# Performance work log

Hardware: AMD Instinct MI355X
Metric: run time of the kernel (lower is better)

The kernel has to match this reference:

```python
import jax, jax.numpy as jnp
import numpy as np


def _gcn_conv(x, W, b, src, dst, num_nodes):
    """PyG GCNConv: linear transform, add self-loops, symmetric norm, scatter-add."""
    h = x @ W  # [N, out] - transform first (cheaper gather on small dim)
    loop = jnp.arange(num_nodes, dtype=src.dtype)
    s = jnp.concatenate([src, loop])  # sources (message senders)
    d = jnp.concatenate([dst, loop])  # targets (aggregators)
    deg = jax.ops.segment_sum(jnp.ones_like(d, dtype=h.dtype), d, num_segments=num_nodes)
    dinv = jnp.where(deg > 0, jax.lax.rsqrt(deg), 0.0)
    norm = dinv[s] * dinv[d]  # [E+N]
    msg = h[s] * norm[:, None]  # gather + scale
    out = jax.ops.segment_sum(msg, d, num_segments=num_nodes)  # scatter-add
    return out + b


def setup_inputs() -> dict:
    key = jax.random.key(0)
    k1, k2, k3, k4 = jax.random.split(key, 4)
    N, F_IN, H, C, E = 100000, 128, 16, 7, 3200000
    x = jax.random.normal(k1, (N, F_IN), dtype=jnp.float32)
    edge_index = jax.random.randint(k2, (2, E), 0, N, dtype=jnp.int64)
    W1 = jax.random.normal(k3, (F_IN, H), dtype=jnp.float32) / np.sqrt(F_IN)
    b1 = jnp.zeros((H,), dtype=jnp.float32)
    W2 = jax.random.normal(k4, (H, C), dtype=jnp.float32) / np.sqrt(H)
    b2 = jnp.zeros((C,), dtype=jnp.float32)
    return {"x": x, "edge_index": edge_index, "W1": W1, "b1": b1, "W2": W2, "b2": b2}


def reference(x, edge_index, W1, b1, W2, b2):
    N = x.shape[0]
    src, dst = edge_index[0], edge_index[1]
    h = _gcn_conv(x, W1, b1, src, dst, N)
    h = jax.nn.relu(h)
    # dropout is identity in eval mode
    h = _gcn_conv(h, W2, b2, src, dst, N)
    return jax.nn.log_softmax(h, axis=1)
```

## Files before the change

### kernel.cpp

```cpp
#include <hip/hip_runtime.h>

#define BSHIFT 7
#define BNODES 128
#define BMASK 127
#define CAP 6144
#define PT 512
#define P_EPB (PT * 16)
#define TPB 256

__device__ __forceinline__ unsigned pkbf2(float a, float b) {
    unsigned ua = __float_as_uint(a), ub = __float_as_uint(b);
    ua = (ua + 0x7fffu + ((ua >> 16) & 1u)) >> 16;
    ub = (ub + 0x7fffu + ((ub >> 16) & 1u)) >> 16;
    return ua | (ub << 16);
}
__device__ __forceinline__ float bflo(unsigned u) { return __uint_as_float(u << 16); }
__device__ __forceinline__ float bfhi(unsigned u) { return __uint_as_float(u & 0xffff0000u); }

__global__ void detect_kernel(const unsigned int* __restrict__ w, int* __restrict__ flag,
                              int* __restrict__ gcur, int nb) {
    __shared__ int any;
    if (threadIdx.x == 0) any = 0;
    __syncthreads();
    int nz = 0;
    for (int k = threadIdx.x; k < 1024; k += blockDim.x)
        if (w[2 * k + 1] != 0u) nz = 1;
    if (nz) atomicOr(&any, 1);
    for (int i = threadIdx.x; i < nb; i += blockDim.x) gcur[i] = 0;
    __syncthreads();
    if (threadIdx.x == 0) *flag = (any == 0) ? 1 : 0;
}

__global__ __launch_bounds__(PT) void fused_place_gemm_kernel(
    const void* __restrict__ ei, const int* __restrict__ flag,
    int* __restrict__ gcur, unsigned* __restrict__ pairs,
    const float* __restrict__ x, const float* __restrict__ W1,
    float* __restrict__ hs, int E, int nb, int pb, int N) {
    __shared__ alignas(16) char smem[47120];
    int tid = threadIdx.x;
    if ((int)blockIdx.x < pb) {
        int* cnt  = (int*)smem;
        int* bbs  = (int*)(smem + 4096);
        int* cur  = (int*)(smem + 8208);
        int* ssum = (int*)(smem + 12304);
        unsigned* stage = (unsigned*)(smem + 14352);
        const bool is64 = (*flag != 0);
        const long long* e64 = (const long long*)ei;
        const int* e32 = (const int*)ei;
        int e0 = blockIdx.x * P_EPB;
        int tot = E - e0; if (tot > P_EPB) tot = P_EPB;
        for (int b = tid; b < nb; b += PT) cnt[b] = 0;
        __syncthreads();
        unsigned pk[16];
        int bk[16];
#pragma unroll
        for (int k = 0; k < 16; ++k) {
            int i = tid + k * PT;
            bk[k] = -1;
            if (i < tot) {
                int e = e0 + i;
                int s, d;
                if (is64) { s = (int)e64[e]; d = (int)e64[E + e]; }
                else      { s = e32[e];      d = e32[E + e]; }
                int b = d >> BSHIFT;
                bk[k] = b;
                pk[k] = ((unsigned)s << BSHIFT) | (unsigned)(d & BMASK);
                atomicAdd(&cnt[b], 1);
            }
        }
        __syncthreads();
        int t2 = tid * 2;
        int c0 = (t2 < nb) ? cnt[t2] : 0;
        int c1 = (t2 + 1 < nb) ? cnt[t2 + 1] : 0;
        int ts = c0 + c1;
        ssum[tid] = ts;
        __syncthreads();
        for (int off = 1; off < PT; off <<= 1) {
            int v = (tid >= off) ? ssum[tid - off] : 0;
            __syncthreads();
            ssum[tid] += v;
            __syncthreads();
        }
        int excl = ssum[tid] - ts;
        if (tid == PT - 1) bbs[nb] = ssum[PT - 1];
        int gb0 = 0, gb1 = 0;
        if (t2 < nb && c0) gb0 = atomicAdd(&gcur[t2], c0);
        if (t2 + 1 < nb && c1) gb1 = atomicAdd(&gcur[t2 + 1], c1);
        if (t2 < nb)     { bbs[t2] = excl;          cnt[t2] = gb0;     cur[t2] = 0; }
        if (t2 + 1 < nb) { bbs[t2 + 1] = excl + c0; cnt[t2 + 1] = gb1; cur[t2 + 1] = 0; }
        __syncthreads();
#pragma unroll
        for (int k = 0; k < 16; ++k) {
            if (bk[k] >= 0) {
                int r = atomicAdd(&cur[bk[k]], 1);
                stage[bbs[bk[k]] + r] = pk[k];
            }
        }
        __syncthreads();
        for (int i = tid; i < tot; i += PT) {
            int lo = 0, hi = nb;
            while (hi - lo > 1) { int mid = (lo + hi) >> 1; if (bbs[mid] <= i) lo = mid; else hi = mid; }
            int slot = cnt[lo] + (i - bbs[lo]);
            if (slot < CAP) pairs[(size_t)lo * CAP + slot] = stage[i];
        }
    } else {
        float* Ws = (float*)smem;
        for (int i = tid; i < 2048; i += PT) Ws[i] = W1[i];
        __syncthreads();
        int n = ((int)blockIdx.x - pb) * PT + tid;
        if (n >= N) return;
        const float4* xp = (const float4*)(x + (size_t)n * 128);
        float a[16];
#pragma unroll
        for (int j = 0; j < 16; ++j) a[j] = 0.f;
#pragma unroll 4
        for (int k4 = 0; k4 < 32; ++k4) {
            float4 xv = xp[k4];
            const float* wr = &Ws[k4 * 64];
#pragma unroll
            for (int j = 0; j < 16; ++j) a[j] += xv.x * wr[j];
#pragma unroll
            for (int j = 0; j < 16; ++j) a[j] += xv.y * wr[16 + j];
#pragma unroll
            for (int j = 0; j < 16; ++j) a[j] += xv.z * wr[32 + j];
#pragma unroll
            for (int j = 0; j < 16; ++j) a[j] += xv.w * wr[48 + j];
        }
        float4* hp = (float4*)(hs + (size_t)n * 16);
#pragma unroll
        for (int j4 = 0; j4 < 4; ++j4) {
            float4 v;
            v.x = a[j4 * 4 + 0]; v.y = a[j4 * 4 + 1];
            v.z = a[j4 * 4 + 2]; v.w = a[j4 * 4 + 3];
            hp[j4] = v;
        }
    }
}

__global__ __launch_bounds__(1024) void scanb_kernel(const int* __restrict__ gcur,
                                                     int* __restrict__ bbase, int nb) {
    __shared__ int sh[1024];
    int t = threadIdx.x;
    int v = 0;
    if (t < nb) { v = gcur[t]; if (v > CAP) v = CAP; }
    sh[t] = v;
    __syncthreads();
    for (int off = 1; off < 1024; off <<= 1) {
        int u = (t >= off) ? sh[t - off] : 0;
        __syncthreads();
        sh[t] += u;
        __syncthreads();
    }
    if (t < nb) bbase[t] = sh[t] - v;
}

__global__ __launch_bounds__(TPB) void csr_build_kernel(
    const unsigned* __restrict__ pairs, const int* __restrict__ gcur,
    const int* __restrict__ bbase, int* __restrict__ csr,
    int* __restrict__ row, int* __restrict__ degA,
    const float* __restrict__ hs1f, uint4* __restrict__ hs1b, int N) {
    __shared__ int hist[BNODES];
    __shared__ int sc[BNODES];
    __shared__ int cur[BNODES];
    __shared__ int stage[CAP];
    int tid = threadIdx.x;
    int b = blockIdx.x;
    if (tid < BNODES) hist[tid] = 0;
    __syncthreads();
    int cnt = gcur[b]; if (cnt > CAP) cnt = CAP;
    int base = bbase[b];
    const unsigned* sl = pairs + (size_t)b * CAP;
    for (int i = tid; i < cnt; i += TPB)
        atomicAdd(&hist[sl[i] & BMASK], 1);
    __syncthreads();
    if (tid < BNODES) sc[tid] = hist[tid];
    __syncthreads();
    for (int off = 1; off < BNODES; off <<= 1) {
        int u = (tid < BNODES && tid >= off) ? sc[tid - off] : 0;
        __syncthreads();
        if (tid < BNODES) sc[tid] += u;
        __syncthreads();
    }
    if (tid < BNODES) {
        int excl = sc[tid] - hist[tid];
        sc[tid] = excl;
        cur[tid] = 0;
        int node = (b << BSHIFT) + tid;
        if (node < N) {
            row[node]  = base + excl;
            degA[node] = hist[tid];
        }
    }
    __syncthreads();
    for (int i = tid; i < cnt; i += TPB) {
        unsigned val = sl[i];
        int l = val & BMASK;
        int r = atomicAdd(&cur[l], 1);
        stage[sc[l] + r] = (int)(val >> BSHIFT);
    }
    __syncthreads();
    for (int i = tid; i < cnt; i += TPB)
        csr[base + i] = stage[i];
    int nodeBase = b << BSHIFT;
    {
        int ln = tid >> 1, half = tid & 1;
        int node = nodeBase + ln;
        if (node < N) {
            float s = rsqrtf((float)(hist[ln] + 1));
            const float4* F = (const float4*)(hs1f + (size_t)node * 16);
            float4 f0 = F[half * 2], f1 = F[half * 2 + 1];
            uint4 u;
            u.x = pkbf2(f0.x * s, f0.y * s); u.y = pkbf2(f0.z * s, f0.w * s);
            u.z = pkbf2(f1.x * s, f1.y * s); u.w = pkbf2(f1.z * s, f1.w * s);
            hs1b[(size_t)node * 2 + half] = u;
        }
    }
}

__global__ __launch_bounds__(TPB) void agg1_kernel(
    const uint4* __restrict__ hs1b, const int* __restrict__ csr,
    const int* __restrict__ row, const int* __restrict__ degA,
    const float* __restrict__ W2, const float* __restrict__ b1,
    uint4* __restrict__ hs2b, int N) {
    __shared__ float Ws[112];
    __shared__ float bs[16];
    int tid = threadIdx.x;
    if (tid < 112) Ws[tid] = W2[tid];
    if (tid < 16) bs[tid] = b1[tid];
    __syncthreads();
    int g = blockIdx.x * TPB + tid;
    int n = g >> 2, quarter = g & 3;
    int st = 0, cnt = 0;
    if (n < N) { st = row[n]; cnt = degA[n]; }
    float acc[16];
#pragma unroll
    for (int j = 0; j < 16; ++j) acc[j] = 0.f;
    int i = st + quarter, end = st + cnt;
    for (; i + 4 < end; i += 8) {
        int s0 = csr[i], s1 = csr[i + 4];
        uint4 g0 = hs1b[(size_t)s0 * 2], g1 = hs1b[(size_t)s0 * 2 + 1];
        uint4 h0 = hs1b[(size_t)s1 * 2], h1 = hs1b[(size_t)s1 * 2 + 1];
        acc[0]  += bflo(g0.x) + bflo(h0.x); acc[1]  += bfhi(g0.x) + bfhi(h0.x);
        acc[2]  += bflo(g0.y) + bflo(h0.y); acc[3]  += bfhi(g0.y) + bfhi(h0.y);
        acc[4]  += bflo(g0.z) + bflo(h0.z); acc[5]  += bfhi(g0.z) + bfhi(h0.z);
        acc[6]  += bflo(g0.w) + bflo(h0.w); acc[7]  += bfhi(g0.w) + bfhi(h0.w);
        acc[8]  += bflo(g1.x) + bflo(h1.x); acc[9]  += bfhi(g1.x) + bfhi(h1.x);
        acc[10] += bflo(g1.y) + bflo(h1.y); acc[11] += bfhi(g1.y) + bfhi(h1.y);
        acc[12] += bflo(g1.z) + bflo(h1.z); acc[13] += bfhi(g1.z) + bfhi(h1.z);
        acc[14] += bflo(g1.w) + bflo(h1.w); acc[15] += bfhi(g1.w) + bfhi(h1.w);
    }
    if (i < end) {
        int s0 = csr[i];
        uint4 g0 = hs1b[(size_t)s0 * 2], g1 = hs1b[(size_t)s0 * 2 + 1];
        acc[0]  += bflo(g0.x); acc[1]  += bfhi(g0.x);
        acc[2]  += bflo(g0.y); acc[3]  += bfhi(g0.y);
        acc[4]  += bflo(g0.z); acc[5]  += bfhi(g0.z);
        acc[6]  += bflo(g0.w); acc[7]  += bfhi(g0.w);
        acc[8]  += bflo(g1.x); acc[9]  += bfhi(g1.x);
        acc[10] += bflo(g1.y); acc[11] += bfhi(g1.y);
        acc[12] += bflo(g1.z); acc[13] += bfhi(g1.z);
        acc[14] += bflo(g1.w); acc[15] += bfhi(g1.w);
    }
#pragma unroll
    for (int j = 0; j < 16; ++j) {
        acc[j] += __shfl_xor(acc[j], 1);
        acc[j] += __shfl_xor(acc[j], 2);
    }
    if (quarter == 0 && n < N) {
        float sc = rsqrtf((float)(cnt + 1));
        uint4 sA = hs1b[(size_t)n * 2], sB = hs1b[(size_t)n * 2 + 1];
        float self[16] = {bflo(sA.x), bfhi(sA.x), bflo(sA.y), bfhi(sA.y),
                          bflo(sA.z), bfhi(sA.z), bflo(sA.w), bfhi(sA.w),
                          bflo(sB.x), bfhi(sB.x), bflo(sB.y), bfhi(sB.y),
                          bflo(sB.z), bfhi(sB.z), bflo(sB.w), bfhi(sB.w)};
        float v[16];
#pragma unroll
        for (int j = 0; j < 16; ++j)
            v[j] = fmaxf(0.f, sc * (acc[j] + self[j]) + bs[j]);
        float h[7];
#pragma unroll
        for (int j = 0; j < 7; ++j) h[j] = 0.f;
#pragma unroll
        for (int k = 0; k < 16; ++k)
#pragma unroll
            for (int j = 0; j < 7; ++j) h[j] += v[k] * Ws[k * 7 + j];
        uint4 u;
        u.x = pkbf2(h[0] * sc, h[1] * sc);
        u.y = pkbf2(h[2] * sc, h[3] * sc);
        u.z = pkbf2(h[4] * sc, h[5] * sc);
        u.w = pkbf2(h[6] * sc, 0.f);
        hs2b[n] = u;
    }
}

__global__ __launch_bounds__(TPB) void agg2_kernel(
    const uint4* __restrict__ hs2b, const int* __restrict__ csr,
    const int* __restrict__ row, const int* __restrict__ degA,
    const float* __restrict__ b2, float* __restrict__ out, int N) {
    __shared__ float bs[8];
    if (threadIdx.x < 7) bs[threadIdx.x] = b2[threadIdx.x];
    __syncthreads();
    int g = blockIdx.x * TPB + threadIdx.x;
    int n = g >> 2, quarter = g & 3;
    int st = 0, cnt = 0;
    if (n < N) { st = row[n]; cnt = degA[n]; }
    float acc[7];
#pragma unroll
    for (int j = 0; j < 7; ++j) acc[j] = 0.f;
    int i = st + quarter, end = st + cnt;
    for (; i + 4 < end; i += 8) {
        int s0 = csr[i], s1 = csr[i + 4];
        uint4 q = hs2b[s0];
        uint4 r = hs2b[s1];
        acc[0] += bflo(q.x) + bflo(r.x); acc[1] += bfhi(q.x) + bfhi(r.x);
        acc[2] += bflo(q.y) + bflo(r.y); acc[3] += bfhi(q.y) + bfhi(r.y);
        acc[4] += bflo(q.z) + bflo(r.z); acc[5] += bfhi(q.z) + bfhi(r.z);
        acc[6] += bflo(q.w) + bflo(r.w);
    }
    if (i < end) {
        uint4 q = hs2b[csr[i]];
        acc[0] += bflo(q.x); acc[1] += bfhi(q.x);
        acc[2] += bflo(q.y); acc[3] += bfhi(q.y);
        acc[4] += bflo(q.z); acc[5] += bfhi(q.z);
        acc[6] += bflo(q.w);
    }
#pragma unroll
    for (int j = 0; j < 7; ++j) {
        acc[j] += __shfl_xor(acc[j], 1);
        acc[j] += __shfl_xor(acc[j], 2);
    }
    if (quarter == 0 && n < N) {
        float sc = rsqrtf((float)(cnt + 1));
        uint4 q = hs2b[n];
        float self[7] = {bflo(q.x), bfhi(q.x), bflo(q.y), bfhi(q.y),
                         bflo(q.z), bfhi(q.z), bflo(q.w)};
        float v[7];
#pragma unroll
        for (int j = 0; j < 7; ++j)
            v[j] = sc * (acc[j] + self[j]) + bs[j];
        float m = v[0];
#pragma unroll
        for (int j = 1; j < 7; ++j) m = fmaxf(m, v[j]);
        float ssum = 0.f;
#pragma unroll
        for (int j = 0; j < 7; ++j) ssum += __expf(v[j] - m);
        float l = m + __logf(ssum);
        float* op = out + (size_t)n * 7;
#pragma unroll
        for (int j = 0; j < 7; ++j) op[j] = v[j] - l;
    }
}

extern "C" void kernel_launch(void* const* d_in, const int* in_sizes, int n_in,
                              void* d_out, int out_size, void* d_ws, size_t ws_size,
                              hipStream_t stream) {
    const float* x  = (const float*)d_in[0];
    const void*  ei = d_in[1];
    const float* W1 = (const float*)d_in[2];
    const float* b1 = (const float*)d_in[3];
    const float* W2 = (const float*)d_in[4];
    const float* b2 = (const float*)d_in[5];
    float* out = (float*)d_out;

    const int Hh  = in_sizes[3];
    const int Fin = in_sizes[2] / Hh;
    const int N   = in_sizes[0] / Fin;
    const long long twoE = in_sizes[1];
    const int E = (int)(twoE / 2);
    const int nb = (N + BNODES - 1) >> BSHIFT;
    (void)n_in; (void)out_size; (void)ws_size;

    char* p = (char*)d_ws;
    auto alloc = [&](size_t bytes) {
        char* r = p;
        p += (bytes + 63) & ~(size_t)63;
        return r;
    };
    int*      flag  = (int*)alloc(sizeof(int));
    int*      gcur  = (int*)alloc(sizeof(int) * (size_t)nb);
    int*      bbase = (int*)alloc(sizeof(int) * 1024);
    unsigned* pairs = (unsigned*)alloc(sizeof(unsigned) * (size_t)nb * CAP);
    int*      csr   = (int*)alloc(sizeof(int) * (size_t)E);
    int*      rowA  = (int*)alloc(sizeof(int) * (size_t)N);
    int*      degA  = (int*)alloc(sizeof(int) * (size_t)N);
    float*    hs1f  = (float*)alloc(sizeof(float) * (size_t)N * 16);
    uint4*    hs1b  = (uint4*)alloc(32 * (size_t)N);
    uint4*    hs2b  = (uint4*)alloc(16 * (size_t)N);

    const int pb = (E + P_EPB - 1) / P_EPB;
    const int gb = (N + PT - 1) / PT;

    detect_kernel<<<1, 256, 0, stream>>>((const unsigned int*)ei, flag, gcur, nb);
    fused_place_gemm_kernel<<<pb + gb, PT, 0, stream>>>(
        ei, flag, gcur, pairs, x, W1, hs1f, E, nb, pb, N);
    scanb_kernel<<<1, 1024, 0, stream>>>(gcur, bbase, nb);
    csr_build_kernel<<<nb, TPB, 0, stream>>>(pairs, gcur, bbase, csr, rowA, degA, hs1f, hs1b, N);
    int aggBlk = (4 * N + TPB - 1) / TPB;
    agg1_kernel<<<aggBlk, TPB, 0, stream>>>(hs1b, csr, rowA, degA, W2, b1, hs2b, N);
    agg2_kernel<<<aggBlk, TPB, 0, stream>>>(hs2b, csr, rowA, degA, b2, out, N);
}
```

Baseline: 119.7 us.

## Drop detect and scan kernels, use padded CSR, bf16 GEMM output, wider agg2

Removes the detect kernel (the int64 check moves into each placement block) and the bucket-scan kernel by laying the CSR out at fixed per-bucket offsets of CAP, and replaces the zeroing with a memset. The placement block shrinks to 256 threads with 4096 edges, uses a wave-shuffle scan, and stores a per-slot bucket id in place of the binary search. The GEMM writes bf16 instead of fp32 to halve that traffic, and agg2 uses 8 lanes per node instead of 4. The cost is a larger padded CSR buffer, a redundant int64 probe in every block, and an extra bf16 rounding before normalization.

```diff
diff --git a/kernel.cpp b/kernel.cpp
--- a/kernel.cpp
+++ b/kernel.cpp
@@ -4,8 +4,8 @@
 #define BNODES 128
 #define BMASK 127
 #define CAP 6144
-#define PT 512
-#define P_EPB (PT * 16)
+#define PT 256
+#define EPB 4096
 #define TPB 256
 
 __device__ __forceinline__ unsigned pkbf2(float a, float b) {
@@ -17,40 +17,35 @@
 __device__ __forceinline__ float bflo(unsigned u) { return __uint_as_float(u << 16); }
 __device__ __forceinline__ float bfhi(unsigned u) { return __uint_as_float(u & 0xffff0000u); }
 
-__global__ void detect_kernel(const unsigned int* __restrict__ w, int* __restrict__ flag,
-                              int* __restrict__ gcur, int nb) {
-    __shared__ int any;
-    if (threadIdx.x == 0) any = 0;
-    __syncthreads();
-    int nz = 0;
-    for (int k = threadIdx.x; k < 1024; k += blockDim.x)
-        if (w[2 * k + 1] != 0u) nz = 1;
-    if (nz) atomicOr(&any, 1);
-    for (int i = threadIdx.x; i < nb; i += blockDim.x) gcur[i] = 0;
-    __syncthreads();
-    if (threadIdx.x == 0) *flag = (any == 0) ? 1 : 0;
-}
-
 __global__ __launch_bounds__(PT) void fused_place_gemm_kernel(
-    const void* __restrict__ ei, const int* __restrict__ flag,
+    const void* __restrict__ ei,
     int* __restrict__ gcur, unsigned* __restrict__ pairs,
     const float* __restrict__ x, const float* __restrict__ W1,
-    float* __restrict__ hs, int E, int nb, int pb, int N) {
-    __shared__ alignas(16) char smem[47120];
+    uint4* __restrict__ hs1u, int E, int nb, int pb, int N) {
+    __shared__ alignas(16) char smem[37120];
     int tid = threadIdx.x;
     if ((int)blockIdx.x < pb) {
         int* cnt  = (int*)smem;
         int* bbs  = (int*)(smem + 4096);
-        int* cur  = (int*)(smem + 8208);
-        int* ssum = (int*)(smem + 12304);
-        unsigned* stage = (unsigned*)(smem + 14352);
-        const bool is64 = (*flag != 0);
+        int* cur  = (int*)(smem + 8192);
+        int* ssum = (int*)(smem + 12288);
+        unsigned* stage = (unsigned*)(smem + 12544);
+        unsigned short* bko = (unsigned short*)(smem + 28928);
+
+        for (int i = tid; i < 1024; i += PT) cnt[i] = 0;
+        if (tid == 0) ssum[8] = 0;
+        const unsigned* w = (const unsigned*)ei;
+        int nz = 0;
+        for (int k = tid; k < 1024; k += PT)
+            if (w[2 * k + 1]) nz = 1;
+        __syncthreads();
+        if (nz) atomicOr(&ssum[8], 1);
+        __syncthreads();
+        const bool is64 = (ssum[8] == 0);
         const long long* e64 = (const long long*)ei;
         const int* e32 = (const int*)ei;
-        int e0 = blockIdx.x * P_EPB;
-        int tot = E - e0; if (tot > P_EPB) tot = P_EPB;
-        for (int b = tid; b < nb; b += PT) cnt[b] = 0;
-        __syncthreads();
+        int e0 = (int)blockIdx.x * EPB;
+        int tot = E - e0; if (tot > EPB) tot = EPB;
         unsigned pk[16];
         int bk[16];
 #pragma unroll
@@ -69,39 +64,53 @@
             }
         }
         __syncthreads();
-        int t2 = tid * 2;
-        int c0 = (t2 < nb) ? cnt[t2] : 0;
-        int c1 = (t2 + 1 < nb) ? cnt[t2 + 1] : 0;
-        int ts = c0 + c1;
-        ssum[tid] = ts;
-        __syncthreads();
-        for (int off = 1; off < PT; off <<= 1) {
-            int v = (tid >= off) ? ssum[tid - off] : 0;
-            __syncthreads();
-            ssum[tid] += v;
-            __syncthreads();
-        }
-        int excl = ssum[tid] - ts;
-        if (tid == PT - 1) bbs[nb] = ssum[PT - 1];
-        int gb0 = 0, gb1 = 0;
-        if (t2 < nb && c0) gb0 = atomicAdd(&gcur[t2], c0);
-        if (t2 + 1 < nb && c1) gb1 = atomicAdd(&gcur[t2 + 1], c1);
-        if (t2 < nb)     { bbs[t2] = excl;          cnt[t2] = gb0;     cur[t2] = 0; }
-        if (t2 + 1 < nb) { bbs[t2 + 1] = excl + c0; cnt[t2 + 1] = gb1; cur[t2 + 1] = 0; }
+        int b0 = tid * 4;
+        int c0 = cnt[b0], c1 = cnt[b0 + 1], c2 = cnt[b0 + 2], c3 = cnt[b0 + 3];
+        int t = c0 + c1 + c2 + c3;
+        int v = t;
+#pragma unroll
+        for (int off = 1; off < 64; off <<= 1) {
+            int u = __shfl_up(v, off);
+            if ((tid & 63) >= off) v += u;
+        }
+        if ((tid & 63) == 63) ssum[tid >> 6] = v;
+        __syncthreads();
+        if (tid == 0) {
+            int r = 0;
+#pragma unroll
+            for (int wv = 0; wv < 4; ++wv) { int xx = ssum[wv]; ssum[wv] = r; r += xx; }
+        }
+        __syncthreads();
+        int excl = v - t + ssum[tid >> 6];
+        int cs[4] = {c0, c1, c2, c3};
+        int run = excl;
+#pragma unroll
+        for (int j = 0; j < 4; ++j) {
+            int b = b0 + j;
+            if (b < nb) {
+                bbs[b] = run;
+                int gb = cs[j] ? atomicAdd(&gcur[b], cs[j]) : 0;
+                cnt[b] = gb;
+                cur[b] = 0;
+            }
+            run += cs[j];
+        }
         __syncthreads();
 #pragma unroll
         for (int k = 0; k < 16; ++k) {
             if (bk[k] >= 0) {
-                int r = atomicAdd(&cur[bk[k]], 1);
-                stage[bbs[bk[k]] + r] = pk[k];
+                int b = bk[k];
+                int r = atomicAdd(&cur[b], 1);
+                int pos = bbs[b] + r;
+                stage[pos] = pk[k];
+                bko[pos] = (unsigned short)b;
             }
         }
         __syncthreads();
         for (int i = tid; i < tot; i += PT) {
-            int lo = 0, hi = nb;
-            while (hi - lo > 1) { int mid = (lo + hi) >> 1; if (bbs[mid] <= i) lo = mid; else hi = mid; }
-            int slot = cnt[lo] + (i - bbs[lo]);
-            if (slot < CAP) pairs[(size_t)lo * CAP + slot] = stage[i];
+            int b = bko[i];
+            int slot = cnt[b] + (i - bbs[b]);
+            if (slot < CAP) pairs[(size_t)b * CAP + slot] = stage[i];
         }
     } else {
         float* Ws = (float*)smem;
@@ -126,39 +135,20 @@
 #pragma unroll
             for (int j = 0; j < 16; ++j) a[j] += xv.w * wr[48 + j];
         }
-        float4* hp = (float4*)(hs + (size_t)n * 16);
-#pragma unroll
-        for (int j4 = 0; j4 < 4; ++j4) {
-            float4 v;
-            v.x = a[j4 * 4 + 0]; v.y = a[j4 * 4 + 1];
-            v.z = a[j4 * 4 + 2]; v.w = a[j4 * 4 + 3];
-            hp[j4] = v;
-        }
-    }
-}
-
-__global__ __launch_bounds__(1024) void scanb_kernel(const int* __restrict__ gcur,
-                                                     int* __restrict__ bbase, int nb) {
-    __shared__ int sh[1024];
-    int t = threadIdx.x;
-    int v = 0;
-    if (t < nb) { v = gcur[t]; if (v > CAP) v = CAP; }
-    sh[t] = v;
-    __syncthreads();
-    for (int off = 1; off < 1024; off <<= 1) {
-        int u = (t >= off) ? sh[t - off] : 0;
-        __syncthreads();
-        sh[t] += u;
-        __syncthreads();
-    }
-    if (t < nb) bbase[t] = sh[t] - v;
+        uint4 u0, u1;
+        u0.x = pkbf2(a[0], a[1]);   u0.y = pkbf2(a[2], a[3]);
+        u0.z = pkbf2(a[4], a[5]);   u0.w = pkbf2(a[6], a[7]);
+        u1.x = pkbf2(a[8], a[9]);   u1.y = pkbf2(a[10], a[11]);
+        u1.z = pkbf2(a[12], a[13]); u1.w = pkbf2(a[14], a[15]);
+        hs1u[(size_t)n * 2]     = u0;
+        hs1u[(size_t)n * 2 + 1] = u1;
+    }
 }
 
 __global__ __launch_bounds__(TPB) void csr_build_kernel(
     const unsigned* __restrict__ pairs, const int* __restrict__ gcur,
-    const int* __restrict__ bbase, int* __restrict__ csr,
-    int* __restrict__ row, int* __restrict__ degA,
-    const float* __restrict__ hs1f, uint4* __restrict__ hs1b, int N) {
+    int* __restrict__ csr, int* __restrict__ row, int* __restrict__ degA,
+    const uint4* __restrict__ hs1u, uint4* __restrict__ hs1b, int N) {
     __shared__ int hist[BNODES];
     __shared__ int sc[BNODES];
     __shared__ int cur[BNODES];
@@ -168,7 +158,7 @@
     if (tid < BNODES) hist[tid] = 0;
     __syncthreads();
     int cnt = gcur[b]; if (cnt > CAP) cnt = CAP;
-    int base = bbase[b];
+    int base = b * CAP;
     const unsigned* sl = pairs + (size_t)b * CAP;
     for (int i = tid; i < cnt; i += TPB)
         atomicAdd(&hist[sl[i] & BMASK], 1);
@@ -201,18 +191,18 @@
     __syncthreads();
     for (int i = tid; i < cnt; i += TPB)
         csr[base + i] = stage[i];
-    int nodeBase = b << BSHIFT;
     {
         int ln = tid >> 1, half = tid & 1;
-        int node = nodeBase + ln;
+        int node = (b << BSHIFT) + ln;
         if (node < N) {
             float s = rsqrtf((float)(hist[ln] + 1));
-            const float4* F = (const float4*)(hs1f + (size_t)node * 16);
-            float4 f0 = F[half * 2], f1 = F[half * 2 + 1];
-            uint4 u;
-            u.x = pkbf2(f0.x * s, f0.y * s); u.y = pkbf2(f0.z * s, f0.w * s);
-            u.z = pkbf2(f1.x * s, f1.y * s); u.w = pkbf2(f1.z * s, f1.w * s);
-            hs1b[(size_t)node * 2 + half] = u;
+            uint4 uu = hs1u[(size_t)node * 2 + half];
+            uint4 o;
+            o.x = pkbf2(bflo(uu.x) * s, bfhi(uu.x) * s);
+            o.y = pkbf2(bflo(uu.y) * s, bfhi(uu.y) * s);
+            o.z = pkbf2(bflo(uu.z) * s, bfhi(uu.z) * s);
+            o.w = pkbf2(bflo(uu.w) * s, bfhi(uu.w) * s);
+            hs1b[(size_t)node * 2 + half] = o;
         }
     }
 }
@@ -301,15 +291,15 @@
     if (threadIdx.x < 7) bs[threadIdx.x] = b2[threadIdx.x];
     __syncthreads();
     int g = blockIdx.x * TPB + threadIdx.x;
-    int n = g >> 2, quarter = g & 3;
+    int n = g >> 3, oct = g & 7;
     int st = 0, cnt = 0;
     if (n < N) { st = row[n]; cnt = degA[n]; }
     float acc[7];
 #pragma unroll
     for (int j = 0; j < 7; ++j) acc[j] = 0.f;
-    int i = st + quarter, end = st + cnt;
-    for (; i + 4 < end; i += 8) {
-        int s0 = csr[i], s1 = csr[i + 4];
+    int i = st + oct, end = st + cnt;
+    for (; i + 8 < end; i += 16) {
+        int s0 = csr[i], s1 = csr[i + 8];
         uint4 q = hs2b[s0];
         uint4 r = hs2b[s1];
         acc[0] += bflo(q.x) + bflo(r.x); acc[1] += bfhi(q.x) + bfhi(r.x);
@@ -328,8 +318,9 @@
     for (int j = 0; j < 7; ++j) {
         acc[j] += __shfl_xor(acc[j], 1);
         acc[j] += __shfl_xor(acc[j], 2);
-    }
-    if (quarter == 0 && n < N) {
+        acc[j] += __shfl_xor(acc[j], 4);
+    }
+    if (oct == 0 && n < N) {
         float sc = rsqrtf((float)(cnt + 1));
         uint4 q = hs2b[n];
         float self[7] = {bflo(q.x), bfhi(q.x), bflo(q.y), bfhi(q.y),
@@ -368,7 +359,7 @@
     const long long twoE = in_sizes[1];
     const int E = (int)(twoE / 2);
     const int nb = (N + BNODES - 1) >> BSHIFT;
-    (void)n_in; (void)out_size; (void)ws_size;
+    (void)n_in; (void)out_size; (void)ws_size; (void)b1;
 
     char* p = (char*)d_ws;
     auto alloc = [&](size_t bytes) {
@@ -376,26 +367,23 @@
         p += (bytes + 63) & ~(size_t)63;
         return r;
     };
-    int*      flag  = (int*)alloc(sizeof(int));
     int*      gcur  = (int*)alloc(sizeof(int) * (size_t)nb);
-    int*      bbase = (int*)alloc(sizeof(int) * 1024);
     unsigned* pairs = (unsigned*)alloc(sizeof(unsigned) * (size_t)nb * CAP);
-    int*      csr   = (int*)alloc(sizeof(int) * (size_t)E);
+    int*      csr   = (int*)alloc(sizeof(int) * (size_t)nb * CAP);
     int*      rowA  = (int*)alloc(sizeof(int) * (size_t)N);
     int*      degA  = (int*)alloc(sizeof(int) * (size_t)N);
-    float*    hs1f  = (float*)alloc(sizeof(float) * (size_t)N * 16);
+    uint4*    hs1u  = (uint4*)alloc(32 * (size_t)N);
     uint4*    hs1b  = (uint4*)alloc(32 * (size_t)N);
     uint4*    hs2b  = (uint4*)alloc(16 * (size_t)N);
 
-    const int pb = (E + P_EPB - 1) / P_EPB;
+    const int pb = (E + EPB - 1) / EPB;
     const int gb = (N + PT - 1) / PT;
 
-    detect_kernel<<<1, 256, 0, stream>>>((const unsigned int*)ei, flag, gcur, nb);
+    hipMemsetAsync(gcur, 0, sizeof(int) * (size_t)nb, stream);
     fused_place_gemm_kernel<<<pb + gb, PT, 0, stream>>>(
-        ei, flag, gcur, pairs, x, W1, hs1f, E, nb, pb, N);
-    scanb_kernel<<<1, 1024, 0, stream>>>(gcur, bbase, nb);
-    csr_build_kernel<<<nb, TPB, 0, stream>>>(pairs, gcur, bbase, csr, rowA, degA, hs1f, hs1b, N);
-    int aggBlk = (4 * N + TPB - 1) / TPB;
-    agg1_kernel<<<aggBlk, TPB, 0, stream>>>(hs1b, csr, rowA, degA, W2, b1, hs2b, N);
-    agg2_kernel<<<aggBlk, TPB, 0, stream>>>(hs2b, csr, rowA, degA, b2, out, N);
-}
+        ei, gcur, pairs, x, W1, hs1u, E, nb, pb, N);
+    csr_build_kernel<<<nb, TPB, 0, stream>>>(pairs, gcur, csr, rowA, degA, hs1u, hs1b, N);
+    agg1_kernel<<<(4 * N + TPB - 1) / TPB, TPB, 0, stream>>>(hs1b, csr, rowA, degA, W2,
+                                                             (const float*)d_in[3], hs2b, N);
+    agg2_kernel<<<(8 * N + TPB - 1) / TPB, TPB, 0, stream>>>(hs2b, csr, rowA, degA, b2, out, N);
+}
```

Measured after the change: 171.1 us. 43.0% more time.
